# Performance work log

Hardware: AMD Instinct MI355X
Metric: run time of the kernel (lower is better)

Reference implementation:

```python
import jax, jax.numpy as jnp
import numpy as np

EPS_GN = 1e-5
EPS_ATTN = 1e-6
HEADS = 4
DIM_HEAD = 32
GROUPS = 32  # min(32, channels=128)


def group_norm(x, weight, bias, groups=GROUPS, eps=EPS_GN):
    # x: [b, c, h, w]
    b, c, h, w = x.shape
    xg = x.reshape(b, groups, c // groups, h, w)
    mean = xg.mean(axis=(2, 3, 4), keepdims=True)
    var = xg.var(axis=(2, 3, 4), keepdims=True)
    xg = (xg - mean) * jax.lax.rsqrt(var + eps)
    x = xg.reshape(b, c, h, w)
    return x * weight[None, :, None, None] + bias[None, :, None, None]


def conv1x1(x, w):
    # x: [b, c, h, w], w: [out, in] -> [b, out, h, w]
    return jnp.einsum('bchw,oc->bohw', x, w)


def setup_inputs() -> dict:
    key = jax.random.key(0)
    ks = jax.random.split(key, 6)
    b, c, h, w = 16, 128, 128, 128
    inner = HEADS * DIM_HEAD  # 128
    x = jax.random.normal(ks[0], (b, c, h, w), dtype=jnp.float32)
    gn1_w = jnp.ones((c,), jnp.float32) + 0.02 * jax.random.normal(ks[1], (c,), jnp.float32)
    gn1_b = 0.02 * jax.random.normal(ks[2], (c,), jnp.float32)
    w_qkv = jax.random.normal(ks[3], (inner * 3, c), jnp.float32) / np.sqrt(c)
    w_out = jax.random.normal(ks[4], (c, inner), jnp.float32) / np.sqrt(inner)
    gn2_w = jnp.ones((c,), jnp.float32) + 0.02 * jax.random.normal(ks[5], (c,), jnp.float32)
    gn2_b = jnp.zeros((c,), jnp.float32)
    return {"x": x, "gn1_w": gn1_w, "gn1_b": gn1_b, "w_qkv": w_qkv,
            "w_out": w_out, "gn2_w": gn2_w, "gn2_b": gn2_b}


def reference(x, gn1_w, gn1_b, w_qkv, w_out, gn2_w, gn2_b):
    b, c, h, w = x.shape
    residual = x
    xn = group_norm(x, gn1_w, gn1_b)
    qkv = conv1x1(xn, w_qkv)                      # [b, 3*inner, h, w]
    q, k, v = jnp.split(qkv, 3, axis=1)
    # 'b (heads d) h w -> b heads (h w) d'
    def to_tokens(t):
        return t.reshape(b, HEADS, DIM_HEAD, h * w).transpose(0, 1, 3, 2)
    q, k, v = to_tokens(q), to_tokens(k), to_tokens(v)
    q = jax.nn.elu(q) + 1.0
    k = jax.nn.elu(k) + 1.0
    k_sum = k.sum(axis=2)                          # [b, heads, d]
    kv = jnp.einsum('bhnd,bhne->bhde', k, v)       # [b, heads, d, d]
    qk_sum = jnp.einsum('bhnd,bhd->bhn', q, k_sum) # [b, heads, n]
    qkv_out = jnp.einsum('bhnd,bhde->bhne', q, kv) # [b, heads, n, d]
    out = qkv_out / (qk_sum[..., None] + EPS_ATTN)
    # 'b heads (h w) d -> b (heads d) h w'
    out = out.transpose(0, 1, 3, 2).reshape(b, HEADS * DIM_HEAD, h, w)
    out = conv1x1(out, w_out)
    out = group_norm(out, gn2_w, gn2_b)
    return out + residual
```

## Files before the change

kernel.cpp:

```cpp
#include <hip/hip_runtime.h>

#define B_   16
#define C_   128
#define HW_  16384

typedef __attribute__((ext_vector_type(4))) float  floatx4;
typedef __attribute__((ext_vector_type(8))) short  short8;
typedef __attribute__((ext_vector_type(4))) short  short4v;

static __device__ __forceinline__ unsigned short f2bf(float f){
  unsigned int u = __float_as_uint(f);
  u += 0x7FFFu + ((u >> 16) & 1u);
  return (unsigned short)(u >> 16);
}
static __device__ __forceinline__ float bf2f(unsigned short h){
  return __uint_as_float(((unsigned int)h) << 16);
}
static __device__ __forceinline__ float elu1(float v){
  return v > 0.f ? v + 1.f : __expf(v);
}
static __device__ __forceinline__ int keyx(int n){ return ((n >> 1) & 7) ^ ((n >> 4) & 7); }

__global__ __launch_bounds__(512) void k_xprep(const float* __restrict__ x,
    unsigned short* __restrict__ xT, float* __restrict__ gn1part){
  int blk = blockIdx.x;
  int b = blk >> 6, tile = blk & 63;
  int n0 = tile * 256;
  __shared__ unsigned short XS[32768];
  int t = threadIdx.x, w = t >> 6, l = t & 63;
  float sk[4], sk2[4];
  #pragma unroll
  for (int k = 0; k < 4; ++k){ sk[k] = 0.f; sk2[k] = 0.f; }
  #pragma unroll
  for (int k = 0; k < 4; ++k){
    float4 f4[4];
    #pragma unroll
    for (int j = 0; j < 4; ++j){
      int c = 16*w + 4*k + j;
      f4[j] = *(const float4*)(x + ((size_t)(b*128 + c))*HW_ + n0 + 4*l);
    }
    #pragma unroll
    for (int j = 0; j < 4; ++j){
      sk[k]  += f4[j].x + f4[j].y + f4[j].z + f4[j].w;
      sk2[k] += f4[j].x*f4[j].x + f4[j].y*f4[j].y + f4[j].z*f4[j].z + f4[j].w*f4[j].w;
    }
    int c0 = 16*w + 4*k, cs = c0 >> 3, co = c0 & 7;
    #pragma unroll
    for (int i = 0; i < 4; ++i){
      int n = 4*l + i;
      short4v p;
      #pragma unroll
      for (int j = 0; j < 4; ++j) p[j] = (short)f2bf(((const float*)&f4[j])[i]);
      *(short4v*)(XS + n*128 + (((cs ^ keyx(n)) << 3) + co)) = p;
    }
  }
  #pragma unroll
  for (int k = 0; k < 4; ++k){
    float a = sk[k], q = sk2[k];
    #pragma unroll
    for (int o = 32; o; o >>= 1){ a += __shfl_down(a, o); q += __shfl_down(q, o); }
    if (l == 0){
      gn1part[((size_t)blk)*64 + (4*w + k)*2 + 0] = a;
      gn1part[((size_t)blk)*64 + (4*w + k)*2 + 1] = q;
    }
  }
  __syncthreads();
  unsigned short* dst = xT + ((size_t)blk)*32768;
  for (int it = 0; it < 8; ++it){
    int slot = t + it*512;
    *(short8*)(dst + slot*8) = *(const short8*)(XS + slot*8);
  }
}

__global__ __launch_bounds__(64) void k_gn1fin(const float* __restrict__ gn1part,
    float* __restrict__ mean, float* __restrict__ rstd){
  int bg = blockIdx.x;
  int b = bg >> 5, g = bg & 31, l = threadIdx.x;
  const float* p = gn1part + ((size_t)(b*64 + l))*64 + g*2;
  float s = p[0], s2 = p[1];
  #pragma unroll
  for (int o = 32; o; o >>= 1){ s += __shfl_down(s, o); s2 += __shfl_down(s2, o); }
  if (l == 0){
    float m = s * (1.f/65536.f);
    float var = s2 * (1.f/65536.f) - m*m;
    mean[bg] = m; rstd[bg] = rsqrtf(var + 1e-5f);
  }
}

__global__ __launch_bounds__(64) void k_fold(const float* __restrict__ wqkv, const float* __restrict__ wout,
    const float* __restrict__ g1w, const float* __restrict__ g1b,
    const float* __restrict__ mean, const float* __restrict__ rstd,
    unsigned short* __restrict__ wqp, float* __restrict__ bias, unsigned short* __restrict__ woutb){
  int i = blockIdx.x, l = threadIdx.x;
  if (i < 6144){
    int b = i / 384, o = i % 384;
    float bsum = 0.f;
    #pragma unroll
    for (int j = 0; j < 2; ++j){
      int c = l*2 + j, g = c >> 2;
      float m = mean[b*32 + g], r = rstd[b*32 + g];
      float A  = r * g1w[c];
      float Bc = g1b[c] - m * A;
      float wv = wqkv[o*128 + c];
      wqp[((size_t)(b*384 + o))*128 + c] = f2bf(wv * A);
      bsum += wv * Bc;
    }
    #pragma unroll
    for (int o2 = 32; o2; o2 >>= 1) bsum += __shfl_down(bsum, o2);
    if (l == 0) bias[b*384 + o] = bsum;
  } else {
    int r = i - 6144;
    #pragma unroll
    for (int j = 0; j < 2; ++j){ int c = l*2 + j; woutb[r*128 + c] = f2bf(wout[r*128 + c]); }
  }
}

__global__ __launch_bounds__(512) void k_kv(const unsigned short* __restrict__ xT,
    const unsigned short* __restrict__ wqp, const float* __restrict__ bias,
    float* __restrict__ kvpart, float* __restrict__ ksumpart){
  int blk = blockIdx.x;
  int b = blk >> 6;
  __shared__ unsigned short S[32768];
  int t = threadIdx.x, w = t >> 6, lane = t & 63, lr = lane & 15, lk = lane >> 4;
  short8 wfr[2][4]; float biasv[2];
  #pragma unroll
  for (int rt = 0; rt < 2; ++rt){
    int o = 128 + rt*128 + w*16;
    #pragma unroll
    for (int ks = 0; ks < 4; ++ks)
      wfr[rt][ks] = *(const short8*)(wqp + ((size_t)(b*384 + o + lr))*128 + ks*32 + lk*8);
    biasv[rt] = bias[b*384 + o + lr];
  }
  short8 ones;
  #pragma unroll
  for (int j = 0; j < 8; ++j) ones[j] = (short)0x3F80;
  floatx4 accA = {0,0,0,0}, accB = {0,0,0,0}, ksaA = {0,0,0,0}, ksaB = {0,0,0,0};
  for (int half = 0; half < 2; ++half){
    const unsigned short* src = xT + ((size_t)blk)*32768 + half*16384;
    for (int it = 0; it < 4; ++it){
      int slot = t + it*512;
      *(short8*)(S + slot*8) = *(const short8*)(src + slot*8);
    }
    __syncthreads();
    short4v kpk[8], vpk[8];
    for (int ct = 0; ct < 8; ++ct){
      int nr = ct*16 + lr;
      int kn = keyx(nr);
      short8 xfr[4];
      #pragma unroll
      for (int ks = 0; ks < 4; ++ks)
        xfr[ks] = *(const short8*)(S + nr*128 + (((ks*4 + lk) ^ kn) << 3));
      #pragma unroll
      for (int rt = 0; rt < 2; ++rt){
        floatx4 acc = {0.f,0.f,0.f,0.f};
        #pragma unroll
        for (int ks = 0; ks < 4; ++ks)
          acc = __builtin_amdgcn_mfma_f32_16x16x32_bf16(xfr[ks], wfr[rt][ks], acc, 0,0,0);
        short4v pk;
        #pragma unroll
        for (int r = 0; r < 4; ++r){
          float v = acc[r] + biasv[rt];
          if (rt == 0) v = elu1(v);
          pk[r] = (short)f2bf(v);
        }
        if (rt == 0) kpk[ct] = pk; else vpk[ct] = pk;
      }
    }
    __syncthreads();
    #pragma unroll
    for (int ct = 0; ct < 8; ++ct){
      int cimg = w*16 + lr;
      int n0 = ct*16 + lk*4;
      int off = cimg*128 + ((((n0 >> 3) ^ ((cimg >> 1) & 7)) << 3) + (n0 & 7));
      *(short4v*)(S + off)         = kpk[ct];
      *(short4v*)(S + 16384 + off) = vpk[ct];
    }
    __syncthreads();
    #pragma unroll
    for (int j = 0; j < 2; ++j){
      int m = w + 8*j;
      int h = m >> 2, dt = (m >> 1) & 1, et = m & 1;
      int arow = h*32 + dt*16 + lr, brow = h*32 + et*16 + lr;
      int akey = (lr >> 1) & 7;
      #pragma unroll
      for (int ks = 0; ks < 4; ++ks){
        short8 ka = *(const short8*)(S + arow*128 + (((ks*4 + lk) ^ akey) << 3));
        short8 vb = *(const short8*)(S + 16384 + brow*128 + (((ks*4 + lk) ^ akey) << 3));
        if (j == 0){
          accA = __builtin_amdgcn_mfma_f32_16x16x32_bf16(ka, vb, accA, 0,0,0);
          if (et == 0) ksaA = __builtin_amdgcn_mfma_f32_16x16x32_bf16(ka, ones, ksaA, 0,0,0);
        } else {
          accB = __builtin_amdgcn_mfma_f32_16x16x32_bf16(ka, vb, accB, 0,0,0);
          if (et == 0) ksaB = __builtin_amdgcn_mfma_f32_16x16x32_bf16(ka, ones, ksaB, 0,0,0);
        }
      }
    }
    __syncthreads();
  }
  #pragma unroll
  for (int j = 0; j < 2; ++j){
    int m = w + 8*j;
    int h = m >> 2, dt = (m >> 1) & 1, et = m & 1;
    floatx4 acc = j ? accB : accA, ksa = j ? ksaB : ksaA;
    float* kvp = kvpart + ((size_t)(blk*4 + h))*1024;
    #pragma unroll
    for (int r = 0; r < 4; ++r)
      kvp[(dt*16 + lk*4 + r)*32 + et*16 + lr] = acc[r];
    if (et == 0 && lr == 0){
      float* ksp = ksumpart + ((size_t)(blk*4 + h))*32;
      #pragma unroll
      for (int r = 0; r < 4; ++r) ksp[dt*16 + lk*4 + r] = ksa[r];
    }
  }
}

__global__ __launch_bounds__(256) void k_kvmfold(const float* __restrict__ kvpart, const float* __restrict__ ksumpart,
    const unsigned short* __restrict__ woutb, unsigned short* __restrict__ Mb, float* __restrict__ ksumF){
  int bh = blockIdx.x, t = threadIdx.x;
  int b = bh >> 2, h = bh & 3;
  __shared__ float kvL[1024];
  for (int i = t; i < 1024; i += 256){
    float s = 0.f;
    for (int nt = 0; nt < 64; ++nt) s += kvpart[((size_t)((b*64 + nt)*4 + h))*1024 + i];
    kvL[i] = s;
  }
  if (t < 32){
    float s = 0.f;
    for (int nt = 0; nt < 64; ++nt) s += ksumpart[((size_t)((b*64 + nt)*4 + h))*32 + t];
    ksumF[b*128 + h*32 + t] = s;
  }
  __syncthreads();
  int o = t >> 1, d0 = (t & 1)*16;
  float w2row[32];
  #pragma unroll
  for (int e = 0; e < 32; ++e) w2row[e] = bf2f(woutb[o*128 + h*32 + e]);
  for (int dd = 0; dd < 16; ++dd){
    int d = d0 + dd;
    float s = 0.f;
    #pragma unroll
    for (int e = 0; e < 32; ++e) s += w2row[e] * kvL[d*32 + e];
    Mb[((size_t)b)*16384 + o*128 + h*32 + d] = f2bf(s);
  }
}

__global__ __launch_bounds__(512) void k_attn2(const unsigned short* __restrict__ xT,
    const unsigned short* __restrict__ wqp, const float* __restrict__ bias,
    const float* __restrict__ ksumF, const unsigned short* __restrict__ Mb,
    unsigned short* __restrict__ hbT, float* __restrict__ gn2part){
  int blk = blockIdx.x;
  int b = blk >> 7, t128 = blk & 127;
  __shared__ unsigned short S[16384];
  int t = threadIdx.x, w = t >> 6, lane = t & 63, lr = lane & 15, lk = lane >> 4;
  int rg = w & 3, cg = w >> 2;
  const unsigned short* src = xT + ((size_t)(b*64 + (t128 >> 1)))*32768 + (t128 & 1)*16384;
  for (int it = 0; it < 4; ++it){
    int slot = t + it*512;
    *(short8*)(S + slot*8) = *(const short8*)(src + slot*8);
  }
  short8 afr[2][4]; float biasq[2][4], ksL[2][4];
  #pragma unroll
  for (int rtl = 0; rtl < 2; ++rtl){
    int o = rg*32 + rtl*16;
    #pragma unroll
    for (int ks = 0; ks < 4; ++ks)
      afr[rtl][ks] = *(const short8*)(wqp + ((size_t)(b*384 + o + lr))*128 + ks*32 + lk*8);
    #pragma unroll
    for (int r = 0; r < 4; ++r){
      biasq[rtl][r] = bias[b*384 + o + lk*4 + r];
      ksL[rtl][r]   = ksumF[b*128 + o + lk*4 + r];
    }
  }
  __syncthreads();
  short4v qpk[2][4];
  #pragma unroll
  for (int ct = 0; ct < 4; ++ct){
    int nr = cg*64 + ct*16 + lr;
    int kn = keyx(nr);
    short8 bfr[4];
    #pragma unroll
    for (int ks = 0; ks < 4; ++ks)
      bfr[ks] = *(const short8*)(S + nr*128 + (((ks*4 + lk) ^ kn) << 3));
    float qv[2][4];
    #pragma unroll
    for (int rtl = 0; rtl < 2; ++rtl){
      floatx4 acc = {0.f,0.f,0.f,0.f};
      #pragma unroll
      for (int ks = 0; ks < 4; ++ks)
        acc = __builtin_amdgcn_mfma_f32_16x16x32_bf16(afr[rtl][ks], bfr[ks], acc, 0,0,0);
      #pragma unroll
      for (int r = 0; r < 4; ++r) qv[rtl][r] = elu1(acc[r] + biasq[rtl][r]);
    }
    float p = 0.f;
    #pragma unroll
    for (int rtl = 0; rtl < 2; ++rtl)
      #pragma unroll
      for (int r = 0; r < 4; ++r) p += ksL[rtl][r] * qv[rtl][r];
    p += __shfl_xor(p, 16);
    p += __shfl_xor(p, 32);
    float inv = 1.f / (p + 1e-6f);
    #pragma unroll
    for (int rtl = 0; rtl < 2; ++rtl){
      short4v pk;
      #pragma unroll
      for (int r = 0; r < 4; ++r) pk[r] = (short)f2bf(qv[rtl][r] * inv);
      qpk[rtl][ct] = pk;
    }
  }
  short8 afr2[4];
  #pragma unroll
  for (int ks = 0; ks < 4; ++ks)
    afr2[ks] = *(const short8*)(Mb + ((size_t)b)*16384 + (size_t)(w*16 + lr)*128 + ks*32 + lk*8);
  __syncthreads();
  #pragma unroll
  for (int rtl = 0; rtl < 2; ++rtl){
    int c0 = rg*32 + rtl*16 + lk*4;
    #pragma unroll
    for (int ct = 0; ct < 4; ++ct){
      int n = cg*64 + ct*16 + lr;
      *(short4v*)(S + n*128 + ((((c0 >> 3) ^ (n & 7)) << 3) + (c0 & 7))) = qpk[rtl][ct];
    }
  }
  __syncthreads();
  unsigned short* hdst = hbT + ((size_t)blk)*16384;
  float gs[4] = {0,0,0,0}, gq[4] = {0,0,0,0};
  #pragma unroll
  for (int ct = 0; ct < 8; ++ct){
    int nr = ct*16 + lr;
    short8 bfr[4];
    #pragma unroll
    for (int ks = 0; ks < 4; ++ks)
      bfr[ks] = *(const short8*)(S + nr*128 + (((ks*4 + lk) ^ (nr & 7)) << 3));
    floatx4 acc = {0.f,0.f,0.f,0.f};
    #pragma unroll
    for (int ks = 0; ks < 4; ++ks)
      acc = __builtin_amdgcn_mfma_f32_16x16x32_bf16(afr2[ks], bfr[ks], acc, 0,0,0);
    short4v pk;
    #pragma unroll
    for (int r = 0; r < 4; ++r){
      float hv = acc[r];
      pk[r] = (short)f2bf(hv);
      gs[r] += hv; gq[r] += hv*hv;
    }
    *(short4v*)(hdst + (w*8 + ct)*256 + lane*4) = pk;
  }
  #pragma unroll
  for (int m = 1; m < 16; m <<= 1)
    #pragma unroll
    for (int r = 0; r < 4; ++r){ gs[r] += __shfl_xor(gs[r], m); gq[r] += __shfl_xor(gq[r], m); }
  if (lr == 0){
    #pragma unroll
    for (int r = 0; r < 4; ++r){
      int c = w*16 + lk*4 + r;
      gn2part[((size_t)blk*128 + c)*2 + 0] = gs[r];
      gn2part[((size_t)blk*128 + c)*2 + 1] = gq[r];
    }
  }
}

__global__ __launch_bounds__(64) void k_gn2stats(const float* __restrict__ gn2part,
    float* __restrict__ mean, float* __restrict__ rstd){
  int b = blockIdx.x >> 5, g = blockIdx.x & 31;
  int lane = threadIdx.x;
  float s = 0.f, s2 = 0.f;
  #pragma unroll
  for (int rr = 0; rr < 2; ++rr){
    int row = lane + rr*64;
    const float* p = gn2part + ((size_t)(b*128 + row))*256 + g*8;
    #pragma unroll
    for (int j = 0; j < 4; ++j){ s += p[j*2]; s2 += p[j*2 + 1]; }
  }
  #pragma unroll
  for (int o = 32; o; o >>= 1){ s += __shfl_down(s, o); s2 += __shfl_down(s2, o); }
  if (lane == 0){
    float m = s * (1.f/65536.f);
    float var = s2 * (1.f/65536.f) - m*m;
    mean[blockIdx.x] = m; rstd[blockIdx.x] = rsqrtf(var + 1e-5f);
  }
}

__global__ __launch_bounds__(256) void k_final(const unsigned short* __restrict__ hbT,
    const unsigned short* __restrict__ xT, float* __restrict__ out,
    const float* __restrict__ mean, const float* __restrict__ rstd,
    const float* __restrict__ g2w, const float* __restrict__ g2b){
  int blk = blockIdx.x;
  int b = blk >> 7, t128 = blk & 127;
  __shared__ unsigned short HS[16384];
  __shared__ unsigned short XS[16384];
  int t = threadIdx.x;
  const unsigned short* hsrc = hbT + ((size_t)blk)*16384;
  const unsigned short* xsrc = xT + ((size_t)(b*64 + (t128 >> 1)))*32768 + (t128 & 1)*16384;
  for (int it = 0; it < 8; ++it){
    int slot = t + it*256;
    *(short8*)(HS + slot*8) = *(const short8*)(hsrc + slot*8);
    *(short8*)(XS + slot*8) = *(const short8*)(xsrc + slot*8);
  }
  __syncthreads();
  for (int it = 0; it < 8; ++it){
    int idx = t + it*256;
    int c = idx >> 4, oct = idx & 15;
    int bg = b*32 + (c >> 2);
    float m = mean[bg], r = rstd[bg];
    float sc = r * g2w[c], sh = g2b[c] - m * sc;
    int hbase0 = ((c >> 4)*8 + (oct >> 1))*256 + ((c >> 2) & 3)*64 + (oct & 1)*32 + (c & 3);
    float ov[8];
    #pragma unroll
    for (int j = 0; j < 8; ++j){
      int n = oct*8 + j;
      float hv = bf2f(HS[hbase0 + j*4]);
      unsigned short xv = XS[n*128 + ((((c >> 3) ^ keyx(n)) << 3) + (c & 7))];
      ov[j] = hv*sc + sh + bf2f(xv);
    }
    float* op = out + ((size_t)(b*128 + c))*HW_ + t128*128 + oct*8;
    float4 o0, o1;
    o0.x = ov[0]; o0.y = ov[1]; o0.z = ov[2]; o0.w = ov[3];
    o1.x = ov[4]; o1.y = ov[5]; o1.z = ov[6]; o1.w = ov[7];
    *(float4*)op = o0; *(float4*)(op + 4) = o1;
  }
}

extern "C" void kernel_launch(void* const* d_in, const int* in_sizes, int n_in,
                              void* d_out, int out_size, void* d_ws, size_t ws_size,
                              hipStream_t stream){
  const float* x    = (const float*)d_in[0];
  const float* g1w  = (const float*)d_in[1];
  const float* g1b  = (const float*)d_in[2];
  const float* wqkv = (const float*)d_in[3];
  const float* wout = (const float*)d_in[4];
  const float* g2w  = (const float*)d_in[5];
  const float* g2b  = (const float*)d_in[6];
  char* ws = (char*)d_ws;
  (void)in_sizes; (void)n_in; (void)out_size; (void)ws_size;

  float* gn1part  = (float*)(ws + 0);
  float* gn1_mean = (float*)(ws + 262144);
  float* gn1_rstd = (float*)(ws + 264192);
  float* gn2_mean = (float*)(ws + 266240);
  float* gn2_rstd = (float*)(ws + 268288);
  float* bias     = (float*)(ws + 270336);
  unsigned short* woutb = (unsigned short*)(ws + 294912);
  float* ksumF    = (float*)(ws + 327680);
  unsigned short* Mb = (unsigned short*)(ws + 335872);
  unsigned short* wqp = (unsigned short*)(ws + 860160);
  float* ksumpart = (float*)(ws + 2433024);
  float* kvpart   = (float*)(ws + 4194304);
  float* gn2part  = (float*)(ws + 37748736);
  unsigned short* xT  = (unsigned short*)(ws + 46137344);
  unsigned short* hbT = (unsigned short*)(ws + 113246208);

  k_xprep<<<dim3(1024), dim3(512), 0, stream>>>(x, xT, gn1part);
  k_gn1fin<<<dim3(512), dim3(64), 0, stream>>>(gn1part, gn1_mean, gn1_rstd);
  k_fold<<<dim3(6272), dim3(64), 0, stream>>>(wqkv, wout, g1w, g1b, gn1_mean, gn1_rstd, wqp, bias, woutb);
  k_kv<<<dim3(1024), dim3(512), 0, stream>>>(xT, wqp, bias, kvpart, ksumpart);
  k_kvmfold<<<dim3(64), dim3(256), 0, stream>>>(kvpart, ksumpart, woutb, Mb, ksumF);
  k_attn2<<<dim3(2048), dim3(512), 0, stream>>>(xT, wqp, bias, ksumF, Mb, hbT, gn2part);
  k_gn2stats<<<dim3(512), dim3(64), 0, stream>>>(gn2part, gn2_mean, gn2_rstd);
  k_final<<<dim3(2048), dim3(256), 0, stream>>>(hbT, xT, (float*)d_out, gn2_mean, gn2_rstd, g2w, g2b);
}
```

Baseline: 216.1 us.

## Store output-projection tile channel-major and read it directly in final kernel

Swaps the MFMA operand order so each lane holds one channel row, and writes the bf16 output-projection tile as a plain [channel][token] layout. That simplifies the GN2 partial-stat reduction to two shuffles. The final kernel then reads the tile straight from global memory with vector loads instead of staging it through LDS, which halves its shared memory. It also adds a rotation to the residual tile's LDS layout to reduce bank conflicts. The risk is less coalesced global stores in the producer and uncached direct global reads in the final kernel.

```diff
diff --git a/kernel.cpp b/kernel.cpp
--- a/kernel.cpp
+++ b/kernel.cpp
@@ -322,7 +322,7 @@
   }
   __syncthreads();
   unsigned short* hdst = hbT + ((size_t)blk)*16384;
-  float gs[4] = {0,0,0,0}, gq[4] = {0,0,0,0};
+  float s1 = 0.f, s2v = 0.f;
   #pragma unroll
   for (int ct = 0; ct < 8; ++ct){
     int nr = ct*16 + lr;
@@ -333,27 +333,22 @@
     floatx4 acc = {0.f,0.f,0.f,0.f};
     #pragma unroll
     for (int ks = 0; ks < 4; ++ks)
-      acc = __builtin_amdgcn_mfma_f32_16x16x32_bf16(afr2[ks], bfr[ks], acc, 0,0,0);
+      acc = __builtin_amdgcn_mfma_f32_16x16x32_bf16(bfr[ks], afr2[ks], acc, 0,0,0);
     short4v pk;
     #pragma unroll
     for (int r = 0; r < 4; ++r){
       float hv = acc[r];
       pk[r] = (short)f2bf(hv);
-      gs[r] += hv; gq[r] += hv*hv;
-    }
-    *(short4v*)(hdst + (w*8 + ct)*256 + lane*4) = pk;
-  }
-  #pragma unroll
-  for (int m = 1; m < 16; m <<= 1)
-    #pragma unroll
-    for (int r = 0; r < 4; ++r){ gs[r] += __shfl_xor(gs[r], m); gq[r] += __shfl_xor(gq[r], m); }
-  if (lr == 0){
-    #pragma unroll
-    for (int r = 0; r < 4; ++r){
-      int c = w*16 + lk*4 + r;
-      gn2part[((size_t)blk*128 + c)*2 + 0] = gs[r];
-      gn2part[((size_t)blk*128 + c)*2 + 1] = gq[r];
-    }
+      s1 += hv; s2v += hv*hv;
+    }
+    *(short4v*)(hdst + (w*16 + lr)*128 + ct*16 + lk*4) = pk;
+  }
+  s1  += __shfl_xor(s1, 16);  s1  += __shfl_xor(s1, 32);
+  s2v += __shfl_xor(s2v, 16); s2v += __shfl_xor(s2v, 32);
+  if (lane < 16){
+    int c = w*16 + lr;
+    gn2part[((size_t)blk*128 + c)*2 + 0] = s1;
+    gn2part[((size_t)blk*128 + c)*2 + 1] = s2v;
   }
 }
 
@@ -384,31 +379,30 @@
     const float* __restrict__ g2w, const float* __restrict__ g2b){
   int blk = blockIdx.x;
   int b = blk >> 7, t128 = blk & 127;
-  __shared__ unsigned short HS[16384];
   __shared__ unsigned short XS[16384];
   int t = threadIdx.x;
-  const unsigned short* hsrc = hbT + ((size_t)blk)*16384;
   const unsigned short* xsrc = xT + ((size_t)(b*64 + (t128 >> 1)))*32768 + (t128 & 1)*16384;
   for (int it = 0; it < 8; ++it){
     int slot = t + it*256;
-    *(short8*)(HS + slot*8) = *(const short8*)(hsrc + slot*8);
-    *(short8*)(XS + slot*8) = *(const short8*)(xsrc + slot*8);
-  }
-  __syncthreads();
+    int n = slot >> 4, sl = slot & 15;
+    *(short8*)(XS + n*128 + (((sl + (n >> 3)) & 15) << 3)) = *(const short8*)(xsrc + slot*8);
+  }
+  __syncthreads();
+  const unsigned short* hsrc = hbT + (size_t)blk*16384;
   for (int it = 0; it < 8; ++it){
     int idx = t + it*256;
     int c = idx >> 4, oct = idx & 15;
     int bg = b*32 + (c >> 2);
     float m = mean[bg], r = rstd[bg];
     float sc = r * g2w[c], sh = g2b[c] - m * sc;
-    int hbase0 = ((c >> 4)*8 + (oct >> 1))*256 + ((c >> 2) & 3)*64 + (oct & 1)*32 + (c & 3);
+    short8 hv = *(const short8*)(hsrc + c*128 + oct*8);
     float ov[8];
     #pragma unroll
     for (int j = 0; j < 8; ++j){
       int n = oct*8 + j;
-      float hv = bf2f(HS[hbase0 + j*4]);
-      unsigned short xv = XS[n*128 + ((((c >> 3) ^ keyx(n)) << 3) + (c & 7))];
-      ov[j] = hv*sc + sh + bf2f(xv);
+      int sl = (c >> 3) ^ keyx(n);
+      unsigned short xv = XS[n*128 + ((((sl + (n >> 3)) & 15) << 3) + (c & 7))];
+      ov[j] = bf2f((unsigned short)hv[j])*sc + sh + bf2f(xv);
     }
     float* op = out + ((size_t)(b*128 + c))*HW_ + t128*128 + oct*8;
     float4 o0, o1;
```

After: 213.8 us. Within noise of the previous version (-1.0%).
